# Kernel tuning notes

Hardware: AMD Instinct MI355X
Metric: run time of the kernel (lower is better)

Reference implementation:

```python
import jax, jax.numpy as jnp
import numpy as np

DT = 0.02
Z_DIM = 32
U_DIM = 16


def _mlp(x, layers):
    # layers: list of (W, b); SiLU between all but last layer
    n = len(layers)
    for i, (W, b) in enumerate(layers):
        x = x @ W + b
        if i < n - 1:
            x = jax.nn.silu(x)
    return x


def _forward(x, u,
             e_w1, e_b1, e_w2, e_b2, e_w3, e_b3,
             d_w1, d_b1, d_w2, d_b2, d_w3, d_b3, d_w4, d_b4,
             a_w1, a_b1, a_w2, a_b2, a_w3, a_b3,
             b_w1, b_b1, b_w2, b_b2, b_w3, b_b3):
    # encode
    z = _mlp(x, [(e_w1, e_b1), (e_w2, e_b2), (e_w3, e_b3)])          # (B, Z)
    # state-dependent A(x) parameters: pairs (a_i, b_i) per 2x2 block
    aux = _mlp(x, [(a_w1, a_b1), (a_w2, a_b2), (a_w3, a_b3)])        # (B, Z)
    a = aux[:, 0::2]                                                  # (B, Z/2)
    b = aux[:, 1::2]
    f = jnp.exp(a * DT)
    c = jnp.cos(b * DT)
    s = jnp.sin(b * DT)
    # A(x) @ z without materializing block-diagonal: per-pair rotation-scale
    z0 = z[:, 0::2]
    z1 = z[:, 1::2]
    Az = jnp.stack([f * (c * z0 - s * z1), f * (s * z0 + c * z1)], axis=-1).reshape(z.shape)
    # B(x) @ u
    Bmat = _mlp(x, [(b_w1, b_b1), (b_w2, b_b2), (b_w3, b_b3)]).reshape(-1, Z_DIM, U_DIM)
    Bu = jnp.einsum('bzu,bu->bz', Bmat, u)
    # latent Euler step + decode
    z_next = z + DT * (Az + Bu)
    return _mlp(z_next, [(d_w1, d_b1), (d_w2, d_b2), (d_w3, d_b3), (d_w4, d_b4)])


def setup_inputs() -> dict:
    key = jax.random.key(0)
    ks = iter(jax.random.split(key, 32))
    def w(shape, scale=0.02):
        return jax.random.normal(next(ks), shape, jnp.float32) * scale
    B, X, U, Z, H, A = 16384, 64, 16, 32, 1024, 256
    return {
        'x': jax.random.normal(next(ks), (B, X), jnp.float32),
        'u': jax.random.normal(next(ks), (B, U), jnp.float32),
        'e_w1': w((X, H)), 'e_b1': w((H,)),
        'e_w2': w((H, H)), 'e_b2': w((H,)),
        'e_w3': w((H, Z)), 'e_b3': w((Z,)),
        'd_w1': w((Z, H)), 'd_b1': w((H,)),
        'd_w2': w((H, H)), 'd_b2': w((H,)),
        'd_w3': w((H, H)), 'd_b3': w((H,)),
        'd_w4': w((H, X)), 'd_b4': w((X,)),
        'a_w1': w((X, A)), 'a_b1': w((A,)),
        'a_w2': w((A, A)), 'a_b2': w((A,)),
        'a_w3': w((A, Z)), 'a_b3': w((Z,)),
        'b_w1': w((X, A)), 'b_b1': w((A,)),
        'b_w2': w((A, A)), 'b_b2': w((A,)),
        'b_w3': w((A, Z * U)), 'b_b3': w((Z * U,)),
    }


def reference(x, u,
              e_w1, e_b1, e_w2, e_b2, e_w3, e_b3,
              d_w1, d_b1, d_w2, d_b2, d_w3, d_b3, d_w4, d_b4,
              a_w1, a_b1, a_w2, a_b2, a_w3, a_b3,
              b_w1, b_b1, b_w2, b_b2, b_w3, b_b3):
    return _forward(x, u,
                    e_w1, e_b1, e_w2, e_b2, e_w3, e_b3,
                    d_w1, d_b1, d_w2, d_b2, d_w3, d_b3, d_w4, d_b4,
                    a_w1, a_b1, a_w2, a_b2, a_w3, a_b3,
                    b_w1, b_b1, b_w2, b_b2, b_w3, b_b3)
```

## Files before the change

### kernel.cpp

```cpp
#include <hip/hip_runtime.h>
#include <cstdint>
#include <cstddef>

#define B_SZ 16384
#define X_D  64
#define U_D  16
#define Z_D  32
#define H_D  1024
#define A_D  256
#define DT_C 0.02f

typedef _Float16 f16;
typedef f16   f16x8 __attribute__((ext_vector_type(8)));
typedef f16   f16x4 __attribute__((ext_vector_type(4)));
typedef float f32x4 __attribute__((ext_vector_type(4)));
typedef float f32x16 __attribute__((ext_vector_type(16)));

#define AS1 __attribute__((address_space(1)))
#define AS3 __attribute__((address_space(3)))

__device__ __forceinline__ void gld_lds16(const void* g, void* l) {
    __builtin_amdgcn_global_load_lds((AS1 void*)(g), (AS3 void*)(l), 16, 0, 0);
}

struct GArg {
    const f16*  A;
    const f16*  W;
    const float* bias;
    void*       C;
    int lda, ldc, K;
};
struct GSet { GArg g[3]; int yn0, yn1; };

template<int BM,int BN,int BK,int WM,int WN,bool SILU,int OM>
__launch_bounds__(256)
__global__ void gemm_k(GSet p)
{
    static_assert(OM != 1 || BN == 128, "OM1 repack assumes BN=128");
    int yb = blockIdx.y, gi = 0;
    if (yb >= p.yn0) { yb -= p.yn0; gi = 1; if (yb >= p.yn1) { yb -= p.yn1; gi = 2; } }
    const GArg ga = p.g[gi];

    constexpr int SEGROW = BK / 8;
    constexpr int SMASK  = (SEGROW < 8 ? SEGROW : 8) - 1;
    constexpr int WTM = BM / WM, WTN = BN / WN;
    static_assert(WTM % 32 == 0 && WTN % 32 == 0, "wave tile in 32x32 units");
    constexpr int RM = WTM / 32, RN = WTN / 32;
    constexpr int KS = BK / 16;
    constexpr int ITA = (BM * SEGROW) / 256;
    constexpr int ITB = (BN * SEGROW) / 256;

    constexpr int STAGE_B = (BM + BN) * BK * 2;
    constexpr int CS_B    = (OM == 1) ? BM * BN * 2 : 0;
    constexpr int SMEM_B  = STAGE_B > CS_B ? STAGE_B : CS_B;
    __shared__ __align__(16) char smem[SMEM_B];
    f16* As = (f16*)smem;
    f16* Bs = As + BM * BK;

    const int tid  = threadIdx.x;
    const int lane = tid & 63;
    const int wave = tid >> 6;
    const int wm = wave / WN, wn = wave % WN;
    const int l31 = lane & 31, half = lane >> 5;

    const size_t arow0 = (size_t)blockIdx.x * BM;
    const size_t brow0 = (size_t)yb * BN;
    const int lda = ga.lda, K = ga.K;

    const f16* aptr[ITA];
    const f16* bptr[ITB];
#pragma unroll
    for (int it = 0; it < ITA; ++it) {
        int s = it * 256 + tid;
        int row = s / SEGROW, st = s % SEGROW;
        int sg = st ^ (row & SMASK);
        aptr[it] = ga.A + (arow0 + row) * lda + sg * 8;
    }
#pragma unroll
    for (int it = 0; it < ITB; ++it) {
        int s = it * 256 + tid;
        int row = s / SEGROW, st = s % SEGROW;
        int sg = st ^ (row & SMASK);
        bptr[it] = ga.W + (brow0 + row) * K + sg * 8;
    }

    f32x16 acc[RM][RN];
#pragma unroll
    for (int i = 0; i < RM; ++i)
#pragma unroll
        for (int j = 0; j < RN; ++j)
#pragma unroll
            for (int r = 0; r < 16; ++r) acc[i][j][r] = 0.f;

    for (int k0 = 0; k0 < K; k0 += BK) {
#pragma unroll
        for (int it = 0; it < ITA; ++it) {
            gld_lds16(aptr[it], &As[(it * 256 + tid) * 8]);
            aptr[it] += BK;
        }
#pragma unroll
        for (int it = 0; it < ITB; ++it) {
            gld_lds16(bptr[it], &Bs[(it * 256 + tid) * 8]);
            bptr[it] += BK;
        }
        __syncthreads();

#pragma unroll
        for (int ks = 0; ks < KS; ++ks) {
            f16x8 af[RM], bf[RN];
#pragma unroll
            for (int i = 0; i < RM; ++i) {
                int row = wm * WTM + i * 32 + l31;
                int st  = (ks * 2 + half) ^ (row & SMASK);
                af[i] = *(const f16x8*)&As[(row * SEGROW + st) * 8];
            }
#pragma unroll
            for (int j = 0; j < RN; ++j) {
                int row = wn * WTN + j * 32 + l31;
                int st  = (ks * 2 + half) ^ (row & SMASK);
                bf[j] = *(const f16x8*)&Bs[(row * SEGROW + st) * 8];
            }
#pragma unroll
            for (int i = 0; i < RM; ++i)
#pragma unroll
                for (int j = 0; j < RN; ++j)
                    acc[i][j] = __builtin_amdgcn_mfma_f32_32x32x16_f16(
                        af[i], bf[j], acc[i][j], 0, 0, 0);
        }
        __syncthreads();
    }

    const int rowbL = wm * WTM;
    const int colbL = wn * WTN;

    if constexpr (OM == 1) {
        f16* Cs = (f16*)smem;
#pragma unroll
        for (int j = 0; j < RN; ++j) {
            int colL = colbL + j * 32 + l31;
            float bv = ga.bias[(int)brow0 + colL];
            int chL = colL >> 3, wi = colL & 7;
#pragma unroll
            for (int i = 0; i < RM; ++i) {
#pragma unroll
                for (int r = 0; r < 16; ++r) {
                    int rowL = rowbL + i * 32 + (r & 3) + 8 * (r >> 2) + 4 * half;
                    float v = acc[i][j][r] + bv;
                    if (SILU) v = v / (1.0f + __expf(-v));
                    Cs[rowL * BN + ((chL ^ (rowL & 15)) << 3) + wi] = (f16)v;
                }
            }
        }
        __syncthreads();
        f16* Cout = (f16*)ga.C;
#pragma unroll
        for (int pass = 0; pass < (BM * BN / 8) / 256; ++pass) {
            int s = pass * 256 + tid;
            int rowL = s >> 4;
            int ch = s & 15;
            f16x8 v = *(const f16x8*)&Cs[rowL * BN + ((ch ^ (rowL & 15)) << 3)];
            *(f16x8*)&Cout[(size_t)(arow0 + rowL) * ga.ldc + brow0 + ch * 8] = v;
        }
    } else {
        float* Cout = (float*)ga.C;
#pragma unroll
        for (int j = 0; j < RN; ++j) {
            int col = (int)brow0 + colbL + j * 32 + l31;
            float bv = ga.bias[col];
#pragma unroll
            for (int i = 0; i < RM; ++i) {
#pragma unroll
                for (int r = 0; r < 16; ++r) {
                    int row = (int)arow0 + rowbL + i * 32
                            + (r & 3) + 8 * (r >> 2) + 4 * half;
                    float v = acc[i][j][r] + bv;
                    if (SILU) v = v / (1.0f + __expf(-v));
                    Cout[(size_t)row * ga.ldc + col] = v;
                }
            }
        }
    }
}

__launch_bounds__(256)
__global__ void mid_k(const f16* __restrict__ cc2,
                      const f16* __restrict__ e_w3t, const float* __restrict__ e_b3,
                      const f16* __restrict__ a_w3t, const float* __restrict__ a_b3,
                      const f16* __restrict__ b_w3t, const float* __restrict__ b_b3,
                      const float* __restrict__ u,   f16* __restrict__ znb)
{
    __shared__ __align__(16) f16 As[32 * 64];
    __shared__ __align__(16) f16 Bs[128 * 64];
    __shared__ float zb[32 * 32];
    __shared__ float ab[32 * 32];
    __shared__ float bu[32 * 32];
    __shared__ float ub[32 * 16];

    const int tid  = threadIdx.x;
    const int lane = tid & 63, wave = tid >> 6;
    const int l15 = lane & 15, quad = lane >> 4;
    const int r0 = blockIdx.x * 32;

    ub[tid]       = u[r0 * 16 + tid];
    ub[tid + 256] = u[r0 * 16 + 256 + tid];

#pragma unroll 1
    for (int ph = 0; ph < 2; ++ph) {
        const f16* W    = ph ? a_w3t : e_w3t;
        const float* bs = ph ? a_b3 : e_b3;
        const int K     = ph ? 256 : 1024;
        const int co    = ph ? 1024 : 0;
        float* ob       = ph ? ab : zb;
        f32x4 acc = {0.f, 0.f, 0.f, 0.f};
        for (int k0 = 0; k0 < K; k0 += 64) {
            {
                int row = tid >> 3, sg = (tid & 7) ^ (row & 7);
                gld_lds16(cc2 + (size_t)(r0 + row) * 1536 + co + k0 + sg * 8,
                          &As[tid * 8]);
            }
            {
                int row = tid >> 3, sg = (tid & 7) ^ (row & 7);
                gld_lds16(W + (size_t)row * K + k0 + sg * 8, &Bs[tid * 8]);
            }
            __syncthreads();
#pragma unroll
            for (int kk = 0; kk < 64; kk += 32) {
                int ar = ((wave >> 1) << 4) + l15;
                int ast = ((kk >> 3) + quad) ^ (ar & 7);
                f16x8 af = *(const f16x8*)&As[(ar * 8 + ast) * 8];
                int br = ((wave & 1) << 4) + l15;
                int bst = ((kk >> 3) + quad) ^ (br & 7);
                f16x8 bf = *(const f16x8*)&Bs[(br * 8 + bst) * 8];
                acc = __builtin_amdgcn_mfma_f32_16x16x32_f16(af, bf, acc, 0, 0, 0);
            }
            __syncthreads();
        }
#pragma unroll
        for (int r = 0; r < 4; ++r) {
            int row = ((wave >> 1) << 4) + quad * 4 + r;
            int col = ((wave & 1) << 4) + l15;
            ob[row * 32 + col] = acc[r] + bs[col];
        }
    }

#pragma unroll 1
    for (int ch = 0; ch < 4; ++ch) {
        f32x4 acc[2][2];
#pragma unroll
        for (int i = 0; i < 2; ++i)
#pragma unroll
            for (int j = 0; j < 2; ++j) acc[i][j] = f32x4{0.f, 0.f, 0.f, 0.f};
        for (int k0 = 0; k0 < 256; k0 += 64) {
            {   int row = tid >> 3, sg = (tid & 7) ^ (row & 7);
                gld_lds16(cc2 + (size_t)(r0 + row) * 1536 + 1280 + k0 + sg * 8,
                          &As[tid * 8]);
            }
#pragma unroll
            for (int it = 0; it < 4; ++it) {
                int s = it * 256 + tid;
                int row = s >> 3, sg = (s & 7) ^ (row & 7);
                gld_lds16(b_w3t + (size_t)(ch * 128 + row) * 256 + k0 + sg * 8,
                          &Bs[s * 8]);
            }
            __syncthreads();
#pragma unroll
            for (int kk = 0; kk < 64; kk += 32) {
                f16x8 af[2], bf[2];
#pragma unroll
                for (int i = 0; i < 2; ++i) {
                    int ar = i * 16 + l15;
                    int st = ((kk >> 3) + quad) ^ (ar & 7);
                    af[i] = *(const f16x8*)&As[(ar * 8 + st) * 8];
                }
#pragma unroll
                for (int j = 0; j < 2; ++j) {
                    int br = wave * 32 + j * 16 + l15;
                    int st = ((kk >> 3) + quad) ^ (br & 7);
                    bf[j] = *(const f16x8*)&Bs[(br * 8 + st) * 8];
                }
#pragma unroll
                for (int i = 0; i < 2; ++i)
#pragma unroll
                    for (int j = 0; j < 2; ++j)
                        acc[i][j] = __builtin_amdgcn_mfma_f32_16x16x32_f16(
                            af[i], bf[j], acc[i][j], 0, 0, 0);
            }
            __syncthreads();
        }
#pragma unroll
        for (int j = 0; j < 2; ++j) {
            int colg = ch * 128 + wave * 32 + j * 16 + l15;
            float bv = b_b3[colg];
            int z = colg >> 4;
#pragma unroll
            for (int i = 0; i < 2; ++i) {
#pragma unroll
                for (int r = 0; r < 4; ++r) {
                    int row = i * 16 + quad * 4 + r;
                    float v = (acc[i][j][r] + bv) * ub[row * 16 + l15];
                    v += __shfl_xor(v, 8, 16);
                    v += __shfl_xor(v, 4, 16);
                    v += __shfl_xor(v, 2, 16);
                    v += __shfl_xor(v, 1, 16);
                    if (l15 == 0) bu[row * 32 + z] = v;
                }
            }
        }
    }
    __syncthreads();

#pragma unroll
    for (int t = 0; t < 4; ++t) {
        int idx = t * 256 + tid;
        int row = idx >> 5, z = idx & 31;
        int pb = idx & ~1;
        float a  = ab[pb], b = ab[pb + 1];
        float z0 = zb[pb], z1 = zb[pb + 1];
        float f  = __expf(a * DT_C);
        float c_ = __cosf(b * DT_C);
        float s_ = __sinf(b * DT_C);
        float Az = (z & 1) ? f * (s_ * z0 + c_ * z1) : f * (c_ * z0 - s_ * z1);
        float zc = (z & 1) ? z1 : z0;
        znb[(size_t)(r0 + row) * 32 + z] = (f16)(zc + DT_C * (Az + bu[idx]));
    }
}

struct PrepArgs {
    const float* w[13];
    f16*         wt[13];
    int          K[13];
    int          N[13];
    const float* bsrc[3];
    float*       bias1;
    const float* x;
    f16*         xb;
};

__launch_bounds__(256)
__global__ void prep_k(PrepArgs pa, int ntrans, int ncvt)
{
    int bid = blockIdx.x;
    if (bid < ntrans) {
        int i = 0, t;
        for (;; ++i) {
            t = (pa.K[i] >> 5) * (pa.N[i] >> 5);
            if (bid < t) break;
            bid -= t;
        }
        const int K = pa.K[i], N = pa.N[i];
        const int tn = N >> 5;
        const int k0 = (bid / tn) << 5, n0 = (bid % tn) << 5;
        __shared__ float tbuf[32][33];
        const int tx = threadIdx.x & 31, ty = threadIdx.x >> 5;
        const float* src = pa.w[i];
        f16* dst = pa.wt[i];
#pragma unroll
        for (int r = 0; r < 32; r += 8)
            tbuf[ty + r][tx] = src[(size_t)(k0 + ty + r) * N + n0 + tx];
        __syncthreads();
#pragma unroll
        for (int r = 0; r < 32; r += 8)
            dst[(size_t)(n0 + ty + r) * K + k0 + tx] = (f16)tbuf[tx][ty + r];
    } else if (bid < ntrans + ncvt) {
        int i = ((bid - ntrans) * 256 + threadIdx.x) * 4;
        float4 v = *(const float4*)(pa.x + i);
        f16x4 o = {(f16)v.x, (f16)v.y, (f16)v.z, (f16)v.w};
        *(f16x4*)(pa.xb + i) = o;
    } else {
        int idx = (bid - ntrans - ncvt) * 256 + (int)threadIdx.x;
        float v = (idx < 1024) ? pa.bsrc[0][idx]
                : (idx < 1280) ? pa.bsrc[1][idx - 1024]
                               : pa.bsrc[2][idx - 1280];
        pa.bias1[idx] = v;
    }
}

extern "C" void kernel_launch(void* const* d_in, const int* in_sizes, int n_in,
                              void* d_out, int out_size, void* d_ws, size_t ws_size,
                              hipStream_t stream)
{
    (void)in_sizes; (void)n_in; (void)out_size; (void)ws_size;
    const float* x    = (const float*)d_in[0];
    const float* u    = (const float*)d_in[1];
    const float* e_w1 = (const float*)d_in[2];  const float* e_b1 = (const float*)d_in[3];
    const float* e_w2 = (const float*)d_in[4];  const float* e_b2 = (const float*)d_in[5];
    const float* e_w3 = (const float*)d_in[6];  const float* e_b3 = (const float*)d_in[7];
    const float* d_w1 = (const float*)d_in[8];  const float* d_b1 = (const float*)d_in[9];
    const float* d_w2 = (const float*)d_in[10]; const float* d_b2 = (const float*)d_in[11];
    const float* d_w3 = (const float*)d_in[12]; const float* d_b3 = (const float*)d_in[13];
    const float* d_w4 = (const float*)d_in[14]; const float* d_b4 = (const float*)d_in[15];
    const float* a_w1 = (const float*)d_in[16]; const float* a_b1 = (const float*)d_in[17];
    const float* a_w2 = (const float*)d_in[18]; const float* a_b2 = (const float*)d_in[19];
    const float* a_w3 = (const float*)d_in[20]; const float* a_b3 = (const float*)d_in[21];
    const float* b_w1 = (const float*)d_in[22]; const float* b_b1 = (const float*)d_in[23];
    const float* b_w2 = (const float*)d_in[24]; const float* b_b2 = (const float*)d_in[25];
    const float* b_w3 = (const float*)d_in[26]; const float* b_b3 = (const float*)d_in[27];

    char* p = (char*)d_ws;
    auto alloc = [&](size_t nbytes) -> void* {
        void* r = (void*)p;
        p += (nbytes + 255) & ~(size_t)255;
        return r;
    };
    f16*   xb   = (f16*)  alloc((size_t)B_SZ * X_D * 2);
    f16*   cc1  = (f16*)  alloc((size_t)B_SZ * 1536 * 2);
    f16*   cc2  = (f16*)  alloc((size_t)B_SZ * 1536 * 2);
    f16*   znb  = (f16*)  alloc((size_t)B_SZ * Z_D * 2);
    f16*   h1d  = cc1;
    f16*   h2d  = cc2;
    f16*   h3d  = cc1;
    f16*   W1t   = (f16*)alloc((size_t)1536 * X_D * 2);
    float* bias1 = (float*)alloc(1536 * 4);
    f16* e_w2t = (f16*)alloc((size_t)H_D * H_D * 2);
    f16* e_w3t = (f16*)alloc((size_t)Z_D * H_D * 2);
    f16* d_w1t = (f16*)alloc((size_t)H_D * Z_D * 2);
    f16* d_w2t = (f16*)alloc((size_t)H_D * H_D * 2);
    f16* d_w3t = (f16*)alloc((size_t)H_D * H_D * 2);
    f16* d_w4t = (f16*)alloc((size_t)X_D * H_D * 2);
    f16* a_w2t = (f16*)alloc((size_t)A_D * A_D * 2);
    f16* a_w3t = (f16*)alloc((size_t)Z_D * A_D * 2);
    f16* b_w2t = (f16*)alloc((size_t)A_D * A_D * 2);
    f16* b_w3t = (f16*)alloc((size_t)(Z_D * U_D) * A_D * 2);

    PrepArgs pa;
    const float* ws_[13] = {e_w1, e_w2, e_w3, d_w1, d_w2, d_w3, d_w4,
                            a_w1, a_w2, a_w3, b_w1, b_w2, b_w3};
    f16* wts_[13] = {W1t, e_w2t, e_w3t, d_w1t, d_w2t, d_w3t, d_w4t,
                     W1t + (size_t)1024 * X_D, a_w2t, a_w3t,
                     W1t + (size_t)1280 * X_D, b_w2t, b_w3t};
    int Ks_[13] = {X_D, H_D, H_D, Z_D, H_D, H_D, H_D, X_D, A_D, A_D, X_D, A_D, A_D};
    int Ns_[13] = {H_D, H_D, Z_D, H_D, H_D, H_D, X_D, A_D, A_D, Z_D, A_D, A_D, Z_D*U_D};
    int ntrans = 0;
    for (int i = 0; i < 13; ++i) {
        pa.w[i] = ws_[i]; pa.wt[i] = wts_[i]; pa.K[i] = Ks_[i]; pa.N[i] = Ns_[i];
        ntrans += (Ks_[i] >> 5) * (Ns_[i] >> 5);
    }
    pa.bsrc[0] = e_b1; pa.bsrc[1] = a_b1; pa.bsrc[2] = b_b1;
    pa.bias1 = bias1; pa.x = x; pa.xb = xb;
    const int ncvt = (B_SZ * X_D) / 1024;
    prep_k<<<ntrans + ncvt + 6, 256, 0, stream>>>(pa, ntrans, ncvt);

    auto G = [](const f16* A, const f16* W, const float* bias, void* C,
                int lda, int ldc, int K) {
        GArg g; g.A = A; g.W = W; g.bias = bias; g.C = C;
        g.lda = lda; g.ldc = ldc; g.K = K; return g;
    };
    GSet s;

    s.g[0] = G(xb, W1t, bias1, cc1, X_D, 1536, X_D);
    s.yn0 = 12; s.yn1 = 0;
    gemm_k<128,128,64,2,2,true,1><<<dim3(B_SZ/128, 12), 256, 0, stream>>>(s);

    s.g[0] = G(cc1,        e_w2t, e_b2, cc2,        1536, 1536, H_D);
    s.g[1] = G(cc1 + 1024, a_w2t, a_b2, cc2 + 1024, 1536, 1536, A_D);
    s.g[2] = G(cc1 + 1280, b_w2t, b_b2, cc2 + 1280, 1536, 1536, A_D);
    s.yn0 = 8; s.yn1 = 2;
    gemm_k<128,128,64,2,2,true,1><<<dim3(B_SZ/128, 12), 256, 0, stream>>>(s);

    mid_k<<<B_SZ/32, 256, 0, stream>>>(cc2, e_w3t, e_b3, a_w3t, a_b3,
                                       b_w3t, b_b3, u, znb);

    s.yn0 = 8; s.yn1 = 0;
    s.g[0] = G(znb, d_w1t, d_b1, h1d, Z_D, H_D, Z_D);
    gemm_k<128,128,32,2,2,true,1><<<dim3(B_SZ/128, 8), 256, 0, stream>>>(s);

    s.g[0] = G(h1d, d_w2t, d_b2, h2d, H_D, H_D, H_D);
    gemm_k<128,128,64,2,2,true,1><<<dim3(B_SZ/128, 8), 256, 0, stream>>>(s);

    s.g[0] = G(h2d, d_w3t, d_b3, h3d, H_D, H_D, H_D);
    gemm_k<128,128,64,2,2,true,1><<<dim3(B_SZ/128, 8), 256, 0, stream>>>(s);

    s.g[0] = G(h3d, d_w4t, d_b4, d_out, H_D, X_D, H_D);
    s.yn0 = 1;
    gemm_k<64,64,64,2,2,false,0><<<dim3(B_SZ/64, 1), 256, 0, stream>>>(s);
}
```

Baseline: 365.0 us.

## Fuse low-K first-layer GEMMs into the following GEMM's A-tile producer

Adds a fused kernel that recomputes each first-layer activation tile (K=64 encoder/aux, K=32 decoder) on the fly with MFMA plus bias and SiLU, writing it straight into LDS as the A operand of the next layer's GEMM. This drops two standalone kernels and the write and re-read of the 16384x1536 and 16384x1024 intermediate activations. In exchange, the first-layer product is recomputed once per N-tile column (8 to 12 times), W1 fragments are read from global memory in the inner loop, and the A tile is built with direct LDS stores instead of async global-to-LDS loads.

Measured after the change: 534.7 us. 46.5% more time.

```diff
diff --git a/kernel.cpp b/kernel.cpp
--- a/kernel.cpp
+++ b/kernel.cpp
@@ -24,10 +24,7 @@
 }
 
 struct GArg {
-    const f16*  A;
-    const f16*  W;
-    const float* bias;
-    void*       C;
+    const f16*  A; const f16* W; const float* bias; void* C;
     int lda, ldc, K;
 };
 struct GSet { GArg g[3]; int yn0, yn1; };
@@ -44,7 +41,6 @@
     constexpr int SEGROW = BK / 8;
     constexpr int SMASK  = (SEGROW < 8 ? SEGROW : 8) - 1;
     constexpr int WTM = BM / WM, WTN = BN / WN;
-    static_assert(WTM % 32 == 0 && WTN % 32 == 0, "wave tile in 32x32 units");
     constexpr int RM = WTM / 32, RN = WTN / 32;
     constexpr int KS = BK / 16;
     constexpr int ITA = (BM * SEGROW) / 256;
@@ -73,15 +69,13 @@
     for (int it = 0; it < ITA; ++it) {
         int s = it * 256 + tid;
         int row = s / SEGROW, st = s % SEGROW;
-        int sg = st ^ (row & SMASK);
-        aptr[it] = ga.A + (arow0 + row) * lda + sg * 8;
+        aptr[it] = ga.A + (arow0 + row) * lda + (st ^ (row & SMASK)) * 8;
     }
 #pragma unroll
     for (int it = 0; it < ITB; ++it) {
         int s = it * 256 + tid;
         int row = s / SEGROW, st = s % SEGROW;
-        int sg = st ^ (row & SMASK);
-        bptr[it] = ga.W + (brow0 + row) * K + sg * 8;
+        bptr[it] = ga.W + (brow0 + row) * K + (st ^ (row & SMASK)) * 8;
     }
 
     f32x16 acc[RM][RN];
@@ -156,8 +150,7 @@
 #pragma unroll
         for (int pass = 0; pass < (BM * BN / 8) / 256; ++pass) {
             int s = pass * 256 + tid;
-            int rowL = s >> 4;
-            int ch = s & 15;
+            int rowL = s >> 4, ch = s & 15;
             f16x8 v = *(const f16x8*)&Cs[rowL * BN + ((ch ^ (rowL & 15)) << 3)];
             *(f16x8*)&Cout[(size_t)(arow0 + rowL) * ga.ldc + brow0 + ch * 8] = v;
         }
@@ -179,6 +172,159 @@
                 }
             }
         }
+    }
+}
+
+struct FArg {
+    const f16*  W;
+    const float* bias;
+    f16*        C;
+    const f16*  W1;
+    const float* b1;
+    int aoff, K, ldc;
+};
+struct FSet { FArg g[3]; int yn0, yn1; const f16* X; };
+
+template<int KX>
+__launch_bounds__(256)
+__global__ void fused_k(FSet p)
+{
+    constexpr int BM = 128, BN = 128, BK = 64;
+    constexpr int SEG = 8;
+    constexpr int KS = 4;
+    constexpr int KSX = KX / 16;
+
+    int yb = blockIdx.y, gi = 0;
+    if (yb >= p.yn0) { yb -= p.yn0; gi = 1; if (yb >= p.yn1) { yb -= p.yn1; gi = 2; } }
+    const FArg ga = p.g[gi];
+
+    __shared__ __align__(16) f16 As[BM * BK];
+    __shared__ __align__(16) f16 Bs[BN * BK];
+
+    const int tid  = threadIdx.x;
+    const int lane = tid & 63;
+    const int wave = tid >> 6;
+    const int wm = wave >> 1, wn = wave & 1;
+    const int l31 = lane & 31, half = lane >> 5;
+
+    const size_t arow0 = (size_t)blockIdx.x * BM;
+    const size_t brow0 = (size_t)yb * BN;
+    const int K = ga.K;
+
+    f16x8 xr[KSX];
+    {
+        const f16* xp = p.X + (arow0 + wave * 32 + l31) * KX + half * 8;
+#pragma unroll
+        for (int ks = 0; ks < KSX; ++ks)
+            xr[ks] = *(const f16x8*)(xp + ks * 16);
+    }
+
+    const f16* bptr[4];
+#pragma unroll
+    for (int it = 0; it < 4; ++it) {
+        int s = it * 256 + tid;
+        int row = s >> 3, st = s & 7;
+        bptr[it] = ga.W + (brow0 + row) * K + (st ^ (row & 7)) * 8;
+    }
+    const f16* w1p[2];
+#pragma unroll
+    for (int t = 0; t < 2; ++t)
+        w1p[t] = ga.W1 + (size_t)(ga.aoff + t * 32 + l31) * KX + half * 8;
+    const float* b1p = ga.b1 + ga.aoff;
+
+    f32x16 acc[2][2];
+#pragma unroll
+    for (int i = 0; i < 2; ++i)
+#pragma unroll
+        for (int j = 0; j < 2; ++j)
+#pragma unroll
+            for (int r = 0; r < 16; ++r) acc[i][j][r] = 0.f;
+
+    const int mrow = wave * 32 + l31;
+    for (int k0 = 0; k0 < K; k0 += BK) {
+#pragma unroll
+        for (int it = 0; it < 4; ++it) {
+            gld_lds16(bptr[it], &Bs[(it * 256 + tid) * 8]);
+            bptr[it] += BK;
+        }
+#pragma unroll
+        for (int t = 0; t < 2; ++t) {
+            f16x8 af[KSX];
+#pragma unroll
+            for (int ks = 0; ks < KSX; ++ks)
+                af[ks] = *(const f16x8*)(w1p[t] + ks * 16);
+            w1p[t] += (size_t)64 * KX;
+            f32x16 at;
+#pragma unroll
+            for (int r = 0; r < 16; ++r) at[r] = 0.f;
+#pragma unroll
+            for (int ks = 0; ks < KSX; ++ks)
+                at = __builtin_amdgcn_mfma_f32_32x32x16_f16(af[ks], xr[ks], at, 0, 0, 0);
+#pragma unroll
+            for (int rq = 0; rq < 4; ++rq) {
+                f32x4 bv = *(const f32x4*)(b1p + k0 + t * 32 + 8 * rq + 4 * half);
+                f16x4 w4;
+#pragma unroll
+                for (int c = 0; c < 4; ++c) {
+                    float v = at[rq * 4 + c] + bv[c];
+                    v = v / (1.0f + __expf(-v));
+                    w4[c] = (f16)v;
+                }
+                int blk = (t * 4 + rq) ^ (mrow & 7);
+                *(f16x4*)&As[(mrow * SEG + blk) * 8 + half * 4] = w4;
+            }
+        }
+        __syncthreads();
+
+#pragma unroll
+        for (int ks = 0; ks < KS; ++ks) {
+            f16x8 af[2], bf[2];
+#pragma unroll
+            for (int i = 0; i < 2; ++i) {
+                int row = wm * 64 + i * 32 + l31;
+                int st  = (ks * 2 + half) ^ (row & 7);
+                af[i] = *(const f16x8*)&As[(row * SEG + st) * 8];
+            }
+#pragma unroll
+            for (int j = 0; j < 2; ++j) {
+                int row = wn * 64 + j * 32 + l31;
+                int st  = (ks * 2 + half) ^ (row & 7);
+                bf[j] = *(const f16x8*)&Bs[(row * SEG + st) * 8];
+            }
+#pragma unroll
+            for (int i = 0; i < 2; ++i)
+#pragma unroll
+                for (int j = 0; j < 2; ++j)
+                    acc[i][j] = __builtin_amdgcn_mfma_f32_32x32x16_f16(
+                        af[i], bf[j], acc[i][j], 0, 0, 0);
+        }
+        __syncthreads();
+    }
+
+    f16* Cs = (f16*)As;
+#pragma unroll
+    for (int j = 0; j < 2; ++j) {
+        int colL = wn * 64 + j * 32 + l31;
+        float bv = ga.bias[(int)brow0 + colL];
+        int chL = colL >> 3, wi = colL & 7;
+#pragma unroll
+        for (int i = 0; i < 2; ++i) {
+#pragma unroll
+            for (int r = 0; r < 16; ++r) {
+                int rowL = wm * 64 + i * 32 + (r & 3) + 8 * (r >> 2) + 4 * half;
+                float v = acc[i][j][r] + bv;
+                v = v / (1.0f + __expf(-v));
+                Cs[rowL * BN + ((chL ^ (rowL & 15)) << 3) + wi] = (f16)v;
+            }
+        }
+    }
+    __syncthreads();
+#pragma unroll
+    for (int pass = 0; pass < 8; ++pass) {
+        int s = pass * 256 + tid;
+        int rowL = s >> 4, ch = s & 15;
+        f16x8 v = *(const f16x8*)&Cs[rowL * BN + ((ch ^ (rowL & 15)) << 3)];
+        *(f16x8*)&ga.C[(size_t)(arow0 + rowL) * ga.ldc + brow0 + ch * 8] = v;
     }
 }
 
@@ -213,13 +359,11 @@
         float* ob       = ph ? ab : zb;
         f32x4 acc = {0.f, 0.f, 0.f, 0.f};
         for (int k0 = 0; k0 < K; k0 += 64) {
-            {
-                int row = tid >> 3, sg = (tid & 7) ^ (row & 7);
+            {   int row = tid >> 3, sg = (tid & 7) ^ (row & 7);
                 gld_lds16(cc2 + (size_t)(r0 + row) * 1536 + co + k0 + sg * 8,
                           &As[tid * 8]);
             }
-            {
-                int row = tid >> 3, sg = (tid & 7) ^ (row & 7);
+            {   int row = tid >> 3, sg = (tid & 7) ^ (row & 7);
                 gld_lds16(W + (size_t)row * K + k0 + sg * 8, &Bs[tid * 8]);
             }
             __syncthreads();
@@ -403,12 +547,10 @@
         return r;
     };
     f16*   xb   = (f16*)  alloc((size_t)B_SZ * X_D * 2);
-    f16*   cc1  = (f16*)  alloc((size_t)B_SZ * 1536 * 2);
     f16*   cc2  = (f16*)  alloc((size_t)B_SZ * 1536 * 2);
     f16*   znb  = (f16*)  alloc((size_t)B_SZ * Z_D * 2);
-    f16*   h1d  = cc1;
-    f16*   h2d  = cc2;
-    f16*   h3d  = cc1;
+    f16*   h2d  = (f16*)  alloc((size_t)B_SZ * H_D * 2);
+    f16*   h3d  = (f16*)  alloc((size_t)B_SZ * H_D * 2);
     f16*   W1t   = (f16*)alloc((size_t)1536 * X_D * 2);
     float* bias1 = (float*)alloc(1536 * 4);
     f16* e_w2t = (f16*)alloc((size_t)H_D * H_D * 2);
@@ -440,37 +582,35 @@
     const int ncvt = (B_SZ * X_D) / 1024;
     prep_k<<<ntrans + ncvt + 6, 256, 0, stream>>>(pa, ntrans, ncvt);
 
-    auto G = [](const f16* A, const f16* W, const float* bias, void* C,
-                int lda, int ldc, int K) {
-        GArg g; g.A = A; g.W = W; g.bias = bias; g.C = C;
-        g.lda = lda; g.ldc = ldc; g.K = K; return g;
-    };
-    GSet s;
-
-    s.g[0] = G(xb, W1t, bias1, cc1, X_D, 1536, X_D);
-    s.yn0 = 12; s.yn1 = 0;
-    gemm_k<128,128,64,2,2,true,1><<<dim3(B_SZ/128, 12), 256, 0, stream>>>(s);
-
-    s.g[0] = G(cc1,        e_w2t, e_b2, cc2,        1536, 1536, H_D);
-    s.g[1] = G(cc1 + 1024, a_w2t, a_b2, cc2 + 1024, 1536, 1536, A_D);
-    s.g[2] = G(cc1 + 1280, b_w2t, b_b2, cc2 + 1280, 1536, 1536, A_D);
-    s.yn0 = 8; s.yn1 = 2;
-    gemm_k<128,128,64,2,2,true,1><<<dim3(B_SZ/128, 12), 256, 0, stream>>>(s);
+    {
+        FSet s;
+        s.X = xb;
+        s.g[0] = FArg{e_w2t, e_b2, cc2,        W1t, bias1, 0,    H_D, 1536};
+        s.g[1] = FArg{a_w2t, a_b2, cc2 + 1024, W1t, bias1, 1024, A_D, 1536};
+        s.g[2] = FArg{b_w2t, b_b2, cc2 + 1280, W1t, bias1, 1280, A_D, 1536};
+        s.yn0 = 8; s.yn1 = 2;
+        fused_k<64><<<dim3(B_SZ/128, 12), 256, 0, stream>>>(s);
+    }
 
     mid_k<<<B_SZ/32, 256, 0, stream>>>(cc2, e_w3t, e_b3, a_w3t, a_b3,
                                        b_w3t, b_b3, u, znb);
 
+    {
+        FSet s;
+        s.X = znb;
+        s.g[0] = FArg{d_w2t, d_b2, h2d, d_w1t, d_b1, 0, H_D, H_D};
+        s.g[1] = s.g[0]; s.g[2] = s.g[0];
+        s.yn0 = 8; s.yn1 = 0;
+        fused_k<32><<<dim3(B_SZ/128, 8), 256, 0, stream>>>(s);
+    }
+
+    GSet s;
+    s.g[0] = GArg{h2d, d_w3t, d_b3, h3d, H_D, H_D, H_D};
+    s.g[1] = s.g[0]; s.g[2] = s.g[0];
     s.yn0 = 8; s.yn1 = 0;
-    s.g[0] = G(znb, d_w1t, d_b1, h1d, Z_D, H_D, Z_D);
-    gemm_k<128,128,32,2,2,true,1><<<dim3(B_SZ/128, 8), 256, 0, stream>>>(s);
-
-    s.g[0] = G(h1d, d_w2t, d_b2, h2d, H_D, H_D, H_D);
     gemm_k<128,128,64,2,2,true,1><<<dim3(B_SZ/128, 8), 256, 0, stream>>>(s);
 
-    s.g[0] = G(h2d, d_w3t, d_b3, h3d, H_D, H_D, H_D);
-    gemm_k<128,128,64,2,2,true,1><<<dim3(B_SZ/128, 8), 256, 0, stream>>>(s);
-
-    s.g[0] = G(h3d, d_w4t, d_b4, d_out, H_D, X_D, H_D);
-    s.yn0 = 1;
+    s.g[0] = GArg{h3d, d_w4t, d_b4, d_out, H_D, X_D, H_D};
+    s.yn0 = 1; s.yn1 = 0;
     gemm_k<64,64,64,2,2,false,0><<<dim3(B_SZ/64, 1), 256, 0, stream>>>(s);
 }
```

## Fuse decoder first layer into mid kernel and last layer into preceding GEMM

Applied to the files above, without the earlier changes.

The mid kernel now computes the d_w1 layer (K=32) directly from the latent z_next held in LDS, so the separate znb buffer and a small GEMM launch go away. The final H->64 projection is fused into the d_w3 GEMM epilogue: each 128-column tile multiplies its SiLU output by the matching slice of d_w4 and atomically adds partial sums into an output pre-seeded with the bias. This removes two kernel launches and the h3 round trip through memory. In exchange it adds fp32 atomics across 8 column tiles, which makes the summation order nondeterministic, and it reads d_w4 directly from global memory inside the epilogue.

Measured after the change: 367.7 us. No clear change (+0.7%).

```diff
diff --git a/kernel.cpp b/kernel.cpp
--- a/kernel.cpp
+++ b/kernel.cpp
@@ -24,11 +24,9 @@
 }
 
 struct GArg {
-    const f16*  A;
-    const f16*  W;
-    const float* bias;
-    void*       C;
+    const f16*  A; const f16* W; const float* bias; void* C;
     int lda, ldc, K;
+    const f16*  W4;
 };
 struct GSet { GArg g[3]; int yn0, yn1; };
 
@@ -36,7 +34,7 @@
 __launch_bounds__(256)
 __global__ void gemm_k(GSet p)
 {
-    static_assert(OM != 1 || BN == 128, "OM1 repack assumes BN=128");
+    static_assert((OM != 1 && OM != 3) || BN == 128, "repack assumes BN=128");
     int yb = blockIdx.y, gi = 0;
     if (yb >= p.yn0) { yb -= p.yn0; gi = 1; if (yb >= p.yn1) { yb -= p.yn1; gi = 2; } }
     const GArg ga = p.g[gi];
@@ -44,14 +42,13 @@
     constexpr int SEGROW = BK / 8;
     constexpr int SMASK  = (SEGROW < 8 ? SEGROW : 8) - 1;
     constexpr int WTM = BM / WM, WTN = BN / WN;
-    static_assert(WTM % 32 == 0 && WTN % 32 == 0, "wave tile in 32x32 units");
     constexpr int RM = WTM / 32, RN = WTN / 32;
     constexpr int KS = BK / 16;
     constexpr int ITA = (BM * SEGROW) / 256;
     constexpr int ITB = (BN * SEGROW) / 256;
 
     constexpr int STAGE_B = (BM + BN) * BK * 2;
-    constexpr int CS_B    = (OM == 1) ? BM * BN * 2 : 0;
+    constexpr int CS_B    = (OM == 1 || OM == 3) ? BM * BN * 2 : 0;
     constexpr int SMEM_B  = STAGE_B > CS_B ? STAGE_B : CS_B;
     __shared__ __align__(16) char smem[SMEM_B];
     f16* As = (f16*)smem;
@@ -73,15 +70,13 @@
     for (int it = 0; it < ITA; ++it) {
         int s = it * 256 + tid;
         int row = s / SEGROW, st = s % SEGROW;
-        int sg = st ^ (row & SMASK);
-        aptr[it] = ga.A + (arow0 + row) * lda + sg * 8;
+        aptr[it] = ga.A + (arow0 + row) * lda + (st ^ (row & SMASK)) * 8;
     }
 #pragma unroll
     for (int it = 0; it < ITB; ++it) {
         int s = it * 256 + tid;
         int row = s / SEGROW, st = s % SEGROW;
-        int sg = st ^ (row & SMASK);
-        bptr[it] = ga.W + (brow0 + row) * K + sg * 8;
+        bptr[it] = ga.W + (brow0 + row) * K + (st ^ (row & SMASK)) * 8;
     }
 
     f32x16 acc[RM][RN];
@@ -133,7 +128,7 @@
     const int rowbL = wm * WTM;
     const int colbL = wn * WTN;
 
-    if constexpr (OM == 1) {
+    if constexpr (OM == 1 || OM == 3) {
         f16* Cs = (f16*)smem;
 #pragma unroll
         for (int j = 0; j < RN; ++j) {
@@ -152,14 +147,44 @@
             }
         }
         __syncthreads();
-        f16* Cout = (f16*)ga.C;
-#pragma unroll
-        for (int pass = 0; pass < (BM * BN / 8) / 256; ++pass) {
-            int s = pass * 256 + tid;
-            int rowL = s >> 4;
-            int ch = s & 15;
-            f16x8 v = *(const f16x8*)&Cs[rowL * BN + ((ch ^ (rowL & 15)) << 3)];
-            *(f16x8*)&Cout[(size_t)(arow0 + rowL) * ga.ldc + brow0 + ch * 8] = v;
+        if constexpr (OM == 1) {
+            f16* Cout = (f16*)ga.C;
+#pragma unroll
+            for (int pass = 0; pass < (BM * BN / 8) / 256; ++pass) {
+                int s = pass * 256 + tid;
+                int rowL = s >> 4, ch = s & 15;
+                f16x8 v = *(const f16x8*)&Cs[rowL * BN + ((ch ^ (rowL & 15)) << 3)];
+                *(f16x8*)&Cout[(size_t)(arow0 + rowL) * ga.ldc + brow0 + ch * 8] = v;
+            }
+        } else {
+            f32x16 a2[2];
+#pragma unroll
+            for (int j = 0; j < 2; ++j)
+#pragma unroll
+                for (int r = 0; r < 16; ++r) a2[j][r] = 0.f;
+#pragma unroll
+            for (int ks = 0; ks < 8; ++ks) {
+                int rowL = wave * 32 + l31;
+                int ch = ks * 2 + half;
+                f16x8 af = *(const f16x8*)&Cs[rowL * BN + ((ch ^ (rowL & 15)) << 3)];
+#pragma unroll
+                for (int j = 0; j < 2; ++j) {
+                    int n = j * 32 + l31;
+                    f16x8 bf = *(const f16x8*)(ga.W4 + (size_t)n * 1024
+                                               + brow0 + ks * 16 + half * 8);
+                    a2[j] = __builtin_amdgcn_mfma_f32_32x32x16_f16(af, bf, a2[j], 0, 0, 0);
+                }
+            }
+            float* Cout = (float*)ga.C;
+#pragma unroll
+            for (int j = 0; j < 2; ++j) {
+                int col = j * 32 + l31;
+#pragma unroll
+                for (int r = 0; r < 16; ++r) {
+                    int row = wave * 32 + (r & 3) + 8 * (r >> 2) + 4 * half;
+                    atomicAdd(Cout + (arow0 + row) * 64 + col, a2[j][r]);
+                }
+            }
         }
     } else {
         float* Cout = (float*)ga.C;
@@ -187,7 +212,8 @@
                       const f16* __restrict__ e_w3t, const float* __restrict__ e_b3,
                       const f16* __restrict__ a_w3t, const float* __restrict__ a_b3,
                       const f16* __restrict__ b_w3t, const float* __restrict__ b_b3,
-                      const float* __restrict__ u,   f16* __restrict__ znb)
+                      const f16* __restrict__ d_w1t, const float* __restrict__ d_b1,
+                      const float* __restrict__ u,   f16* __restrict__ h1d)
 {
     __shared__ __align__(16) f16 As[32 * 64];
     __shared__ __align__(16) f16 Bs[128 * 64];
@@ -195,10 +221,12 @@
     __shared__ float ab[32 * 32];
     __shared__ float bu[32 * 32];
     __shared__ float ub[32 * 16];
+    __shared__ f16   zn2[32 * 36];
 
     const int tid  = threadIdx.x;
     const int lane = tid & 63, wave = tid >> 6;
     const int l15 = lane & 15, quad = lane >> 4;
+    const int l31 = lane & 31, half = lane >> 5;
     const int r0 = blockIdx.x * 32;
 
     ub[tid]       = u[r0 * 16 + tid];
@@ -213,13 +241,11 @@
         float* ob       = ph ? ab : zb;
         f32x4 acc = {0.f, 0.f, 0.f, 0.f};
         for (int k0 = 0; k0 < K; k0 += 64) {
-            {
-                int row = tid >> 3, sg = (tid & 7) ^ (row & 7);
+            {   int row = tid >> 3, sg = (tid & 7) ^ (row & 7);
                 gld_lds16(cc2 + (size_t)(r0 + row) * 1536 + co + k0 + sg * 8,
                           &As[tid * 8]);
             }
-            {
-                int row = tid >> 3, sg = (tid & 7) ^ (row & 7);
+            {   int row = tid >> 3, sg = (tid & 7) ^ (row & 7);
                 gld_lds16(W + (size_t)row * K + k0 + sg * 8, &Bs[tid * 8]);
             }
             __syncthreads();
@@ -321,8 +347,47 @@
         float s_ = __sinf(b * DT_C);
         float Az = (z & 1) ? f * (s_ * z0 + c_ * z1) : f * (c_ * z0 - s_ * z1);
         float zc = (z & 1) ? z1 : z0;
-        znb[(size_t)(r0 + row) * 32 + z] = (f16)(zc + DT_C * (Az + bu[idx]));
-    }
+        zn2[row * 36 + z] = (f16)(zc + DT_C * (Az + bu[idx]));
+    }
+    __syncthreads();
+
+#pragma unroll 1
+    for (int nb = 0; nb < 8; ++nb) {
+#pragma unroll
+        for (int it = 0; it < 2; ++it) {
+            int s = it * 256 + tid;
+            int row = s >> 2, sg = (s & 3) ^ (row & 3);
+            gld_lds16(d_w1t + (size_t)(nb * 128 + row) * 32 + sg * 8, &Bs[s * 8]);
+        }
+        __syncthreads();
+        f32x16 a1;
+#pragma unroll
+        for (int r = 0; r < 16; ++r) a1[r] = 0.f;
+        const int nl = wave * 32 + l31;
+#pragma unroll
+        for (int ks = 0; ks < 2; ++ks) {
+            f16x8 af = *(const f16x8*)&zn2[l31 * 36 + ks * 16 + half * 8];
+            f16x8 bf = *(const f16x8*)&Bs[nl * 32 + (((ks * 2 + half) ^ (nl & 3)) << 3)];
+            a1 = __builtin_amdgcn_mfma_f32_32x32x16_f16(af, bf, a1, 0, 0, 0);
+        }
+        float bv = d_b1[nb * 128 + nl];
+#pragma unroll
+        for (int r = 0; r < 16; ++r) {
+            int rowD = (r & 3) + 8 * (r >> 2) + 4 * half;
+            float v = a1[r] + bv;
+            v = v / (1.0f + __expf(-v));
+            h1d[(size_t)(r0 + rowD) * 1024 + nb * 128 + nl] = (f16)v;
+        }
+        __syncthreads();
+    }
+}
+
+__launch_bounds__(256)
+__global__ void seed_k(const float* __restrict__ b4, float* __restrict__ out)
+{
+    int idx = blockIdx.x * 256 + threadIdx.x;
+    float4 bv = *(const float4*)(b4 + ((idx * 4) & 63));
+    *(float4*)(out + (size_t)idx * 4) = bv;
 }
 
 struct PrepArgs {
@@ -405,10 +470,8 @@
     f16*   xb   = (f16*)  alloc((size_t)B_SZ * X_D * 2);
     f16*   cc1  = (f16*)  alloc((size_t)B_SZ * 1536 * 2);
     f16*   cc2  = (f16*)  alloc((size_t)B_SZ * 1536 * 2);
-    f16*   znb  = (f16*)  alloc((size_t)B_SZ * Z_D * 2);
     f16*   h1d  = cc1;
     f16*   h2d  = cc2;
-    f16*   h3d  = cc1;
     f16*   W1t   = (f16*)alloc((size_t)1536 * X_D * 2);
     float* bias1 = (float*)alloc(1536 * 4);
     f16* e_w2t = (f16*)alloc((size_t)H_D * H_D * 2);
@@ -422,6 +485,8 @@
     f16* b_w2t = (f16*)alloc((size_t)A_D * A_D * 2);
     f16* b_w3t = (f16*)alloc((size_t)(Z_D * U_D) * A_D * 2);
 
+    seed_k<<<(B_SZ * X_D) / 1024, 256, 0, stream>>>(d_b4, (float*)d_out);
+
     PrepArgs pa;
     const float* ws_[13] = {e_w1, e_w2, e_w3, d_w1, d_w2, d_w3, d_w4,
                             a_w1, a_w2, a_w3, b_w1, b_w2, b_w3};
@@ -441,13 +506,13 @@
     prep_k<<<ntrans + ncvt + 6, 256, 0, stream>>>(pa, ntrans, ncvt);
 
     auto G = [](const f16* A, const f16* W, const float* bias, void* C,
-                int lda, int ldc, int K) {
+                int lda, int ldc, int K, const f16* W4 = nullptr) {
         GArg g; g.A = A; g.W = W; g.bias = bias; g.C = C;
-        g.lda = lda; g.ldc = ldc; g.K = K; return g;
+        g.lda = lda; g.ldc = ldc; g.K = K; g.W4 = W4; return g;
     };
     GSet s;
 
-    s.g[0] = G(xb, W1t, bias1, cc1, X_D, 1536, X_D);
+    s.g[0] = s.g[1] = s.g[2] = G(xb, W1t, bias1, cc1, X_D, 1536, X_D);
     s.yn0 = 12; s.yn1 = 0;
     gemm_k<128,128,64,2,2,true,1><<<dim3(B_SZ/128, 12), 256, 0, stream>>>(s);
 
@@ -458,19 +523,13 @@
     gemm_k<128,128,64,2,2,true,1><<<dim3(B_SZ/128, 12), 256, 0, stream>>>(s);
 
     mid_k<<<B_SZ/32, 256, 0, stream>>>(cc2, e_w3t, e_b3, a_w3t, a_b3,
-                                       b_w3t, b_b3, u, znb);
-
+                                       b_w3t, b_b3, d_w1t, d_b1, u, h1d);
+
+    s.g[0] = s.g[1] = s.g[2] = G(h1d, d_w2t, d_b2, h2d, H_D, H_D, H_D);
     s.yn0 = 8; s.yn1 = 0;
-    s.g[0] = G(znb, d_w1t, d_b1, h1d, Z_D, H_D, Z_D);
-    gemm_k<128,128,32,2,2,true,1><<<dim3(B_SZ/128, 8), 256, 0, stream>>>(s);
-
-    s.g[0] = G(h1d, d_w2t, d_b2, h2d, H_D, H_D, H_D);
     gemm_k<128,128,64,2,2,true,1><<<dim3(B_SZ/128, 8), 256, 0, stream>>>(s);
 
-    s.g[0] = G(h2d, d_w3t, d_b3, h3d, H_D, H_D, H_D);
-    gemm_k<128,128,64,2,2,true,1><<<dim3(B_SZ/128, 8), 256, 0, stream>>>(s);
-
-    s.g[0] = G(h3d, d_w4t, d_b4, d_out, H_D, X_D, H_D);
-    s.yn0 = 1;
-    gemm_k<64,64,64,2,2,false,0><<<dim3(B_SZ/64, 1), 256, 0, stream>>>(s);
+    s.g[0] = s.g[1] = s.g[2] = G(h2d, d_w3t, d_b3, d_out, H_D, 64, H_D, d_w4t);
+    s.yn0 = 8; s.yn1 = 0;
+    gemm_k<128,128,64,2,2,true,3><<<dim3(B_SZ/128, 8), 256, 0, stream>>>(s);
 }
```
